# Kernel tuning notes

Hardware: AMD Instinct MI355X
Metric: run time of the kernel (lower is better)

Reference implementation:

```python
import jax, jax.numpy as jnp
import numpy as np

N_NODES = 50000
N_EDGES = 800000
IN_DIM = 96
HID_DIM = 96


def setup_inputs() -> dict:
    key = jax.random.key(0)
    ks = jax.random.split(key, 8)
    inputs = jax.random.normal(ks[0], (N_NODES, IN_DIM), dtype=jnp.float32)
    factor = jax.random.uniform(ks[1], (N_EDGES, 1), dtype=jnp.float32)
    src = jax.random.randint(ks[2], (N_EDGES,), 0, N_NODES, dtype=jnp.int32)
    dst = jax.random.randint(ks[3], (N_EDGES,), 0, N_NODES, dtype=jnp.int32)
    # Linear params (torch nn.Linear: y = x @ W.T + b), uniform(-1/sqrt(fan_in), ..)
    s1 = 1.0 / np.sqrt(IN_DIM)
    s2 = 1.0 / np.sqrt(HID_DIM)
    W1 = jax.random.uniform(ks[4], (HID_DIM, IN_DIM), minval=-s1, maxval=s1, dtype=jnp.float32)
    b1 = jax.random.uniform(ks[5], (HID_DIM,), minval=-s1, maxval=s1, dtype=jnp.float32)
    W2 = jax.random.uniform(ks[6], (IN_DIM, HID_DIM), minval=-s2, maxval=s2, dtype=jnp.float32)
    b2 = jax.random.uniform(ks[7], (IN_DIM,), minval=-s2, maxval=s2, dtype=jnp.float32)
    return {"inputs": inputs, "W1": W1, "b1": b1, "W2": W2, "b2": b2,
            "factor": factor, "src": src, "dst": dst}


def _propagate(feat, factor, src, dst, n_nodes):
    # message = h[src] * edge_factor ; reduce = sum at dst
    msg = feat[src] * factor                       # [E, D]
    return jax.ops.segment_sum(msg, dst, num_segments=n_nodes)


def reference(inputs, W1, b1, W2, b2, factor, src, dst):
    n = inputs.shape[0]
    # in-degree norm: deg^{-1/2}, clamped at 1
    deg = jax.ops.segment_sum(jnp.ones((src.shape[0],), inputs.dtype), dst,
                              num_segments=n)
    norm = jnp.maximum(deg, 1.0) ** -0.5           # [N]
    norm = norm[:, None]                           # [N, 1]

    feat = (inputs @ W1.T + b1) * norm             # [N, H]
    h = jnp.tanh(_propagate(feat, factor, src, dst, n))

    feat = (h @ W2.T + b2) * norm                  # [N, D]
    h = jnp.tanh(_propagate(feat, factor, src, dst, n))

    # dgl.mean_nodes over a single graph -> [1, D]; unsqueeze(-1) -> [1, D, 1]
    pooled = jnp.mean(h, axis=0, keepdims=True)[..., None]
    return jnp.tanh(pooled)
```

## Files before the change

### kernel.cpp

```cpp
#include <hip/hip_runtime.h>
#include <math.h>
#include <type_traits>

#define N_NODES 50000
#define N_EDGES 800000
#define DIM 96
#define BCH 12
#define SCAN_BLK 256
#define NBLK ((N_NODES + SCAN_BLK - 1) / SCAN_BLK)
#define NPB 21
#define NBG ((N_NODES + NPB - 1) / NPB)
#define CAP 768
#define R1_ROWS 24
#define R1_BLOCKS ((NBG + R1_ROWS - 1) / R1_ROWS)

typedef short v8s __attribute__((ext_vector_type(8)));
typedef float v4f __attribute__((ext_vector_type(4)));

__device__ __forceinline__ unsigned short f2bf(float f) {
    unsigned int u = __float_as_uint(f);
    u += 0x7FFFu + ((u >> 16) & 1u);
    return (unsigned short)(u >> 16);
}
__device__ __forceinline__ unsigned int pack2bf(float lo, float hi) {
    return (unsigned int)f2bf(lo) | ((unsigned int)f2bf(hi) << 16);
}
__device__ __forceinline__ float bflo(unsigned int u) { return __uint_as_float(u << 16); }
__device__ __forceinline__ float bfhi(unsigned int u) { return __uint_as_float(u & 0xFFFF0000u); }

__device__ __forceinline__ float fast_tanh(float x) {
    float ax = fabsf(x);
    float t = __expf(-2.0f * ax);
    float r = (1.0f - t) / (1.0f + t);
    return copysignf(r, x);
}

__device__ __forceinline__ void acc8(float* a, uint4 v, float f) {
    a[0] += bflo(v.x) * f; a[1] += bfhi(v.x) * f;
    a[2] += bflo(v.y) * f; a[3] += bfhi(v.y) * f;
    a[4] += bflo(v.z) * f; a[5] += bfhi(v.z) * f;
    a[6] += bflo(v.w) * f; a[7] += bfhi(v.w) * f;
}

union U4S8 { uint4 u; v8s s; };


__global__ void link_edges(const int* __restrict__ dst, int* __restrict__ head,
                           int* __restrict__ nxt) {
    int e = blockIdx.x * blockDim.x + threadIdx.x;
    if (e >= N_EDGES) return;
    int old = atomicExch(&head[dst[e]], e);
    nxt[e] = old;
}

__global__ void walk_count_partials(const int* __restrict__ head, const int* __restrict__ nxt,
                                    int* __restrict__ deg, float* __restrict__ norm,
                                    int* __restrict__ partials) {
    int b = blockIdx.x, t = threadIdx.x;
    int n = b * SCAN_BLK + t;
    int cnt = 0;
    if (n < N_NODES) {
        int p = head[n];
        while (p >= 0) { ++cnt; p = nxt[p]; }
        deg[n] = cnt;
        norm[n] = rsqrtf(fmaxf((float)cnt, 1.0f));
    }
    int v = cnt;
#pragma unroll
    for (int off = 32; off > 0; off >>= 1) v += __shfl_down(v, off, 64);
    __shared__ int ws[4];
    if ((t & 63) == 0) ws[t >> 6] = v;
    __syncthreads();
    if (t == 0) partials[b] = ws[0] + ws[1] + ws[2] + ws[3];
}

__global__ void scan_partials(const int* __restrict__ partials, int* __restrict__ pprefix) {
    __shared__ int sm[SCAN_BLK];
    int t = threadIdx.x;
    int v = (t < NBLK) ? partials[t] : 0;
    sm[t] = v;
    __syncthreads();
    for (int off = 1; off < SCAN_BLK; off <<= 1) {
        int u = (t >= off) ? sm[t - off] : 0;
        __syncthreads();
        sm[t] += u;
        __syncthreads();
    }
    if (t < NBLK) pprefix[t] = sm[t] - v;
}

__global__ void scan_compact(const int* __restrict__ deg, const int* __restrict__ pprefix,
                             const int* __restrict__ head, const int* __restrict__ nxt,
                             const int* __restrict__ src, const float* __restrict__ factor,
                             int* __restrict__ offs, int2* __restrict__ entries) {
    __shared__ int sm[SCAN_BLK];
    int b = blockIdx.x, t = threadIdx.x;
    int idx = b * SCAN_BLK + t;
    int v = (idx < N_NODES) ? deg[idx] : 0;
    sm[t] = v;
    __syncthreads();
    for (int off = 1; off < SCAN_BLK; off <<= 1) {
        int u = (t >= off) ? sm[t - off] : 0;
        __syncthreads();
        sm[t] += u;
        __syncthreads();
    }
    if (idx < N_NODES) {
        int o = pprefix[b] + sm[t] - v;
        offs[idx] = o;
        int p = head[idx];
        while (p >= 0) {
            entries[o++] = make_int2(src[p], __float_as_int(factor[p]));
            p = nxt[p];
        }
    }
    if (b == 0 && t == 0) offs[N_NODES] = N_EDGES;
}


__global__ void swizzle_W(const float* __restrict__ W, uint4* __restrict__ bsw) {
    int idx = blockIdx.x * blockDim.x + threadIdx.x;
    if (idx >= 18 * 64) return;
    int t = idx >> 6, lane = idx & 63;
    int kt = t / 6, jt = t % 6;
    int quad = lane >> 4, l16 = lane & 15;
    const float4* wp = (const float4*)(W + (size_t)(jt * 16 + l16) * DIM + kt * 32 + quad * 8);
    float4 w0 = wp[0], w1 = wp[1];
    bsw[idx] = make_uint4(pack2bf(w0.x, w0.y), pack2bf(w0.z, w0.w),
                          pack2bf(w1.x, w1.y), pack2bf(w1.z, w1.w));
}


#define TILE_SH 104

template <typename T>
__global__ __launch_bounds__(256) void gemm_mfma(const T* __restrict__ X,
                                                 const uint4* __restrict__ bsw,
                                                 const float* __restrict__ bias,
                                                 const float* __restrict__ norm,
                                                 unsigned short* __restrict__ out) {
    __shared__ unsigned short tile[4][16 * TILE_SH];
    int tid = threadIdx.x;
    int wave = tid >> 6, lane = tid & 63;
    int quad = lane >> 4, l16 = lane & 15;
    int n0 = blockIdx.x * 64 + wave * 16;
    int rowc = min(n0 + l16, N_NODES - 1);

    uint4 bfr[18];
#pragma unroll
    for (int t = 0; t < 18; ++t) bfr[t] = bsw[t * 64 + lane];

    v4f acc[6];
#pragma unroll
    for (int jt = 0; jt < 6; ++jt) acc[jt] = (v4f)(0.0f);

#pragma unroll
    for (int kt = 0; kt < 3; ++kt) {
        U4S8 a;
        if constexpr (std::is_same_v<T, float>) {
            const float4* xp = (const float4*)(X + (size_t)rowc * DIM + kt * 32 + quad * 8);
            float4 x0 = xp[0], x1 = xp[1];
            a.u = make_uint4(pack2bf(x0.x, x0.y), pack2bf(x0.z, x0.w),
                             pack2bf(x1.x, x1.y), pack2bf(x1.z, x1.w));
        } else {
            a.u = *(const uint4*)(X + (size_t)rowc * DIM + kt * 32 + quad * 8);
        }
#pragma unroll
        for (int jt = 0; jt < 6; ++jt) {
            U4S8 bb; bb.u = bfr[kt * 6 + jt];
            acc[jt] = __builtin_amdgcn_mfma_f32_16x16x32_bf16(a.s, bb.s, acc[jt], 0, 0, 0);
        }
    }

    float nm[4];
#pragma unroll
    for (int r = 0; r < 4; ++r) nm[r] = norm[min(n0 + quad * 4 + r, N_NODES - 1)];
#pragma unroll
    for (int jt = 0; jt < 6; ++jt) {
        float bj = bias[jt * 16 + l16];
#pragma unroll
        for (int r = 0; r < 4; ++r) {
            float v = (acc[jt][r] + bj) * nm[r];
            tile[wave][(quad * 4 + r) * TILE_SH + jt * 16 + l16] = f2bf(v);
        }
    }
    __builtin_amdgcn_s_waitcnt(0);
#pragma unroll
    for (int i = 0; i < 3; ++i) {
        int chunk = lane + 64 * i;
        int rr = chunk / 12, cc = chunk - rr * 12;
        int gn = n0 + rr;
        if (gn < N_NODES) {
            uint4 v = *(uint4*)&tile[wave][rr * TILE_SH + cc * 8];
            *(uint4*)(out + (size_t)gn * DIM + cc * 8) = v;
        }
    }
}


template <bool DO_TANH, bool POOL>
__global__ void gather_agg_bf16(const unsigned short* __restrict__ feat,
                                const int* __restrict__ offs,
                                const int2* __restrict__ entries,
                                unsigned short* __restrict__ out,
                                float* __restrict__ partials) {
    __shared__ int2 ents[CAP];
    __shared__ float pool[DIM];
    __shared__ int sh_base, sh_cnt;
    int tid = threadIdx.x;
    int n0 = blockIdx.x * NPB;
    int n1 = min(n0 + NPB, N_NODES);
    if (POOL && tid < DIM) pool[tid] = 0.f;
    if (tid == 0) { sh_base = offs[n0]; sh_cnt = offs[n1] - sh_base; }
    __syncthreads();
    int base = sh_base, cnt = sh_cnt;

    int nl = tid / BCH;
    int c  = tid - nl * BCH;
    int n  = n0 + nl;
    bool active = (tid < NPB * BCH) && (n < N_NODES);
    int lb = 0, le = 0;
    if (active) { lb = offs[n] - base; le = offs[n + 1] - base; }

    float a0[8], a1[8];
#pragma unroll
    for (int i = 0; i < 8; ++i) { a0[i] = 0.f; a1[i] = 0.f; }

    for (int tb = 0; tb < cnt; tb += CAP) {
        int tcnt = min(cnt - tb, CAP);
        if (tb) __syncthreads();
        for (int i = tid; i < tcnt; i += 256) ents[i] = entries[base + tb + i];
        __syncthreads();
        int s = max(lb - tb, 0), e = min(le - tb, tcnt);
        int p = s;
        for (; p + 3 < e; p += 4) {
            int2 e0 = ents[p], e1 = ents[p + 1], e2 = ents[p + 2], e3 = ents[p + 3];
            uint4 v0 = *((const uint4*)(feat + (size_t)e0.x * DIM) + c);
            uint4 v1 = *((const uint4*)(feat + (size_t)e1.x * DIM) + c);
            uint4 v2 = *((const uint4*)(feat + (size_t)e2.x * DIM) + c);
            uint4 v3 = *((const uint4*)(feat + (size_t)e3.x * DIM) + c);
            acc8(a0, v0, __int_as_float(e0.y));
            acc8(a1, v1, __int_as_float(e1.y));
            acc8(a0, v2, __int_as_float(e2.y));
            acc8(a1, v3, __int_as_float(e3.y));
        }
        for (; p < e; ++p) {
            int2 e0 = ents[p];
            uint4 v0 = *((const uint4*)(feat + (size_t)e0.x * DIM) + c);
            acc8(a0, v0, __int_as_float(e0.y));
        }
    }

#pragma unroll
    for (int i = 0; i < 8; ++i) a0[i] += a1[i];
    if (DO_TANH || POOL) {
#pragma unroll
        for (int i = 0; i < 8; ++i) a0[i] = fast_tanh(a0[i]);
    }
    if (!POOL) {
        if (active) {
            uint4 o;
            o.x = pack2bf(a0[0], a0[1]);
            o.y = pack2bf(a0[2], a0[3]);
            o.z = pack2bf(a0[4], a0[5]);
            o.w = pack2bf(a0[6], a0[7]);
            ((uint4*)out)[n * BCH + c] = o;
        }
    } else {
        if (active) {
#pragma unroll
            for (int i = 0; i < 8; ++i) atomicAdd(&pool[c * 8 + i], a0[i]);
        }
        __syncthreads();
        if (tid < DIM) partials[(size_t)blockIdx.x * DIM + tid] = pool[tid];
    }
}


__global__ void reduce_stage1(const float* __restrict__ poolpart, float* __restrict__ stage1) {
    __shared__ float pool[DIM];
    int b = blockIdx.x, t = threadIdx.x;
    if (t < DIM) pool[t] = 0.f;
    __syncthreads();
    const int base = b * R1_ROWS * DIM;
    float loc = 0.f;
    int lastc = -1;
    for (int i = t; i < R1_ROWS * DIM; i += 256) {
        int gi = base + i;
        if (gi < NBG * DIM) {
            int col = i % DIM;
            if (col != lastc) {
                if (lastc >= 0) atomicAdd(&pool[lastc], loc);
                lastc = col; loc = 0.f;
            }
            loc += poolpart[gi];
        }
    }
    if (lastc >= 0) atomicAdd(&pool[lastc], loc);
    __syncthreads();
    if (t < DIM) stage1[b * DIM + t] = pool[t];
}

__global__ void reduce_stage2(const float* __restrict__ stage1, float* __restrict__ out) {
    __shared__ float sm[960];
    int t = threadIdx.x;
    int col = t % DIM, slice = t / DIM;
    float s = 0.f;
    for (int k = slice; k < R1_BLOCKS; k += 10) s += stage1[k * DIM + col];
    sm[t] = s;
    __syncthreads();
    if (t < DIM) {
        float tot = 0.f;
#pragma unroll
        for (int i = 0; i < 10; ++i) tot += sm[i * DIM + t];
        out[t] = tanhf(tot * (1.0f / N_NODES));
    }
}


extern "C" void kernel_launch(void* const* d_in, const int* in_sizes, int n_in,
                              void* d_out, int out_size, void* d_ws, size_t ws_size,
                              hipStream_t stream) {
    const float* inputs = (const float*)d_in[0];
    const float* W1     = (const float*)d_in[1];
    const float* b1     = (const float*)d_in[2];
    const float* W2     = (const float*)d_in[3];
    const float* b2     = (const float*)d_in[4];
    const float* factor = (const float*)d_in[5];
    const int*   src    = (const int*)d_in[6];
    const int*   dst    = (const int*)d_in[7];
    float* out = (float*)d_out;

    char* ws = (char*)d_ws;
    int*            head     = (int*)(ws + 0);
    int*            nxt      = (int*)(ws + 262144);
    int*            deg      = (int*)(ws + 3670016);
    int*            offs     = (int*)(ws + 3932160);
    float*          norm     = (float*)(ws + 4194304);
    int*            partials = (int*)(ws + 4456448);
    int*            pprefix  = (int*)(ws + 4458496);
    int2*           entries  = (int2*)(ws + 4718592);
    unsigned short* bufA     = (unsigned short*)(ws + 11534336);
    unsigned short* bufB     = (unsigned short*)(ws + 21364736);
    float*          poolpart = (float*)(ws + 31195136);
    float*          stage1   = (float*)(ws + 32145536);
    uint4*          bsw1     = (uint4*)(ws + 33554432);
    uint4*          bsw2     = (uint4*)(ws + 33574912);

    swizzle_W<<<5, 256, 0, stream>>>(W1, bsw1);
    swizzle_W<<<5, 256, 0, stream>>>(W2, bsw2);

    hipMemsetAsync(head, 0xFF, N_NODES * sizeof(int), stream);
    link_edges<<<(N_EDGES + 255) / 256, 256, 0, stream>>>(dst, head, nxt);
    walk_count_partials<<<NBLK, SCAN_BLK, 0, stream>>>(head, nxt, deg, norm, partials);
    scan_partials<<<1, SCAN_BLK, 0, stream>>>(partials, pprefix);
    scan_compact<<<NBLK, SCAN_BLK, 0, stream>>>(deg, pprefix, head, nxt, src, factor,
                                                offs, entries);

    const int GEMM_BLOCKS = (N_NODES + 63) / 64;

    gemm_mfma<float><<<GEMM_BLOCKS, 256, 0, stream>>>(inputs, bsw1, b1, norm, bufA);
    gather_agg_bf16<true, false><<<NBG, 256, 0, stream>>>(bufA, offs, entries, bufB, nullptr);

    gemm_mfma<unsigned short><<<GEMM_BLOCKS, 256, 0, stream>>>(bufB, bsw2, b2, norm, bufA);
    gather_agg_bf16<false, true><<<NBG, 256, 0, stream>>>(bufA, offs, entries, nullptr, poolpart);

    reduce_stage1<<<R1_BLOCKS, 256, 0, stream>>>(poolpart, stage1);
    reduce_stage2<<<1, 960, 0, stream>>>(stage1, out);
}
```

Baseline: 265.0 us.

## Sort nodes by in-degree via histogram bins to balance gather aggregation work

Replaces the prefix-scan CSR build with a degree histogram, a per-bin scan and a rank-assignment pass. Nodes of equal in-degree become contiguous, so each gather block processes nodes with uniform edge counts. The goal is to cut divergence and idle lanes inside waves of the gather kernels. In exchange it adds a preprocessing kernel, atomic rank assignment and scattered output writes through a permutation. Degrees of 256 or more would index past the bin arrays.

```diff
diff --git a/kernel.cpp b/kernel.cpp
--- a/kernel.cpp
+++ b/kernel.cpp
@@ -11,6 +11,7 @@
 #define NPB 21
 #define NBG ((N_NODES + NPB - 1) / NPB)
 #define CAP 768
+#define NBINS 256
 #define R1_ROWS 24
 #define R1_BLOCKS ((NBG + R1_ROWS - 1) / R1_ROWS)
 
@@ -53,68 +54,74 @@
     nxt[e] = old;
 }
 
-__global__ void walk_count_partials(const int* __restrict__ head, const int* __restrict__ nxt,
-                                    int* __restrict__ deg, float* __restrict__ norm,
-                                    int* __restrict__ partials) {
-    int b = blockIdx.x, t = threadIdx.x;
-    int n = b * SCAN_BLK + t;
-    int cnt = 0;
+__global__ void walk_count_hist(const int* __restrict__ head, const int* __restrict__ nxt,
+                                int* __restrict__ deg, float* __restrict__ norm,
+                                int* __restrict__ bins) {
+    __shared__ int h[NBINS];
+    int t = threadIdx.x;
+    h[t] = 0;
+    __syncthreads();
+    int n = blockIdx.x * SCAN_BLK + t;
     if (n < N_NODES) {
+        int cnt = 0;
         int p = head[n];
         while (p >= 0) { ++cnt; p = nxt[p]; }
         deg[n] = cnt;
         norm[n] = rsqrtf(fmaxf((float)cnt, 1.0f));
-    }
-    int v = cnt;
-#pragma unroll
-    for (int off = 32; off > 0; off >>= 1) v += __shfl_down(v, off, 64);
-    __shared__ int ws[4];
-    if ((t & 63) == 0) ws[t >> 6] = v;
-    __syncthreads();
-    if (t == 0) partials[b] = ws[0] + ws[1] + ws[2] + ws[3];
-}
-
-__global__ void scan_partials(const int* __restrict__ partials, int* __restrict__ pprefix) {
-    __shared__ int sm[SCAN_BLK];
+        atomicAdd(&h[min(cnt, NBINS - 1)], 1);
+    }
+    __syncthreads();
+    if (h[t]) atomicAdd(&bins[t], h[t]);
+}
+
+__global__ void bin_scan(const int* __restrict__ bins, int* __restrict__ nodeStart,
+                         int* __restrict__ edgeStart, int* __restrict__ binCursor) {
+    __shared__ int a[NBINS], b[NBINS];
     int t = threadIdx.x;
-    int v = (t < NBLK) ? partials[t] : 0;
-    sm[t] = v;
-    __syncthreads();
-    for (int off = 1; off < SCAN_BLK; off <<= 1) {
-        int u = (t >= off) ? sm[t - off] : 0;
+    int c = bins[t];
+    int cw = c * t;
+    a[t] = c; b[t] = cw;
+    __syncthreads();
+    for (int off = 1; off < NBINS; off <<= 1) {
+        int u = (t >= off) ? a[t - off] : 0;
+        int v = (t >= off) ? b[t - off] : 0;
         __syncthreads();
-        sm[t] += u;
+        a[t] += u; b[t] += v;
         __syncthreads();
     }
-    if (t < NBLK) pprefix[t] = sm[t] - v;
-}
-
-__global__ void scan_compact(const int* __restrict__ deg, const int* __restrict__ pprefix,
-                             const int* __restrict__ head, const int* __restrict__ nxt,
-                             const int* __restrict__ src, const float* __restrict__ factor,
-                             int* __restrict__ offs, int2* __restrict__ entries) {
-    __shared__ int sm[SCAN_BLK];
-    int b = blockIdx.x, t = threadIdx.x;
-    int idx = b * SCAN_BLK + t;
-    int v = (idx < N_NODES) ? deg[idx] : 0;
-    sm[t] = v;
-    __syncthreads();
-    for (int off = 1; off < SCAN_BLK; off <<= 1) {
-        int u = (t >= off) ? sm[t - off] : 0;
-        __syncthreads();
-        sm[t] += u;
-        __syncthreads();
-    }
-    if (idx < N_NODES) {
-        int o = pprefix[b] + sm[t] - v;
-        offs[idx] = o;
-        int p = head[idx];
-        while (p >= 0) {
-            entries[o++] = make_int2(src[p], __float_as_int(factor[p]));
-            p = nxt[p];
-        }
-    }
-    if (b == 0 && t == 0) offs[N_NODES] = N_EDGES;
+    nodeStart[t] = a[t] - c;
+    edgeStart[t] = b[t] - cw;
+    binCursor[t] = 0;
+}
+
+__global__ void rank_assign(const int* __restrict__ deg, const int* __restrict__ nodeStart,
+                            const int* __restrict__ edgeStart, int* __restrict__ binCursor,
+                            int* __restrict__ perm, int* __restrict__ eoffs,
+                            int* __restrict__ soffs) {
+    int n = blockIdx.x * SCAN_BLK + threadIdx.x;
+    if (n < N_NODES) {
+        int d = deg[n];
+        int w = atomicAdd(&binCursor[d], 1);
+        int r = nodeStart[d] + w;
+        int eo = edgeStart[d] + w * d;
+        perm[r] = n;
+        eoffs[n] = eo;
+        soffs[r] = eo;
+    }
+    if (n == 0) soffs[N_NODES] = N_EDGES;
+}
+
+__global__ void compact(const int* __restrict__ head, const int* __restrict__ nxt,
+                        const int* __restrict__ src, const float* __restrict__ factor,
+                        const int* __restrict__ eoffs, int2* __restrict__ entries) {
+    int n = blockIdx.x * SCAN_BLK + threadIdx.x;
+    if (n >= N_NODES) return;
+    int o = eoffs[n];
+    int p = head[n];
+    while (p >= 0) {
+        entries[o++] = make_int2(src[p], __float_as_int(factor[p]));
+        p = nxt[p];
+    }
 }
 
 
@@ -200,7 +207,8 @@
 
 template <bool DO_TANH, bool POOL>
 __global__ void gather_agg_bf16(const unsigned short* __restrict__ feat,
-                                const int* __restrict__ offs,
+                                const int* __restrict__ soffs,
+                                const int* __restrict__ perm,
                                 const int2* __restrict__ entries,
                                 unsigned short* __restrict__ out,
                                 float* __restrict__ partials) {
@@ -208,19 +216,19 @@
     __shared__ float pool[DIM];
     __shared__ int sh_base, sh_cnt;
     int tid = threadIdx.x;
-    int n0 = blockIdx.x * NPB;
-    int n1 = min(n0 + NPB, N_NODES);
+    int r0 = blockIdx.x * NPB;
+    int r1 = min(r0 + NPB, N_NODES);
     if (POOL && tid < DIM) pool[tid] = 0.f;
-    if (tid == 0) { sh_base = offs[n0]; sh_cnt = offs[n1] - sh_base; }
+    if (tid == 0) { sh_base = soffs[r0]; sh_cnt = soffs[r1] - sh_base; }
     __syncthreads();
     int base = sh_base, cnt = sh_cnt;
 
     int nl = tid / BCH;
     int c  = tid - nl * BCH;
-    int n  = n0 + nl;
-    bool active = (tid < NPB * BCH) && (n < N_NODES);
+    int rk = r0 + nl;
+    bool active = (tid < NPB * BCH) && (rk < N_NODES);
     int lb = 0, le = 0;
-    if (active) { lb = offs[n] - base; le = offs[n + 1] - base; }
+    if (active) { lb = soffs[rk] - base; le = soffs[rk + 1] - base; }
 
     float a0[8], a1[8];
 #pragma unroll
@@ -259,12 +267,13 @@
     }
     if (!POOL) {
         if (active) {
+            int n_out = perm[rk];
             uint4 o;
             o.x = pack2bf(a0[0], a0[1]);
             o.y = pack2bf(a0[2], a0[3]);
             o.z = pack2bf(a0[4], a0[5]);
             o.w = pack2bf(a0[6], a0[7]);
-            ((uint4*)out)[n * BCH + c] = o;
+            ((uint4*)out)[n_out * BCH + c] = o;
         }
     } else {
         if (active) {
@@ -332,38 +341,46 @@
     float* out = (float*)d_out;
 
     char* ws = (char*)d_ws;
-    int*            head     = (int*)(ws + 0);
-    int*            nxt      = (int*)(ws + 262144);
-    int*            deg      = (int*)(ws + 3670016);
-    int*            offs     = (int*)(ws + 3932160);
-    float*          norm     = (float*)(ws + 4194304);
-    int*            partials = (int*)(ws + 4456448);
-    int*            pprefix  = (int*)(ws + 4458496);
-    int2*           entries  = (int2*)(ws + 4718592);
-    unsigned short* bufA     = (unsigned short*)(ws + 11534336);
-    unsigned short* bufB     = (unsigned short*)(ws + 21364736);
-    float*          poolpart = (float*)(ws + 31195136);
-    float*          stage1   = (float*)(ws + 32145536);
-    uint4*          bsw1     = (uint4*)(ws + 33554432);
-    uint4*          bsw2     = (uint4*)(ws + 33574912);
+    int*            head      = (int*)(ws + 0);
+    int*            nxt       = (int*)(ws + 262144);
+    int*            deg       = (int*)(ws + 3670016);
+    int*            soffs     = (int*)(ws + 3932160);
+    float*          norm      = (float*)(ws + 4194304);
+    int*            bins      = (int*)(ws + 4456448);
+    int*            nodeStart = (int*)(ws + 4457472);
+    int*            edgeStart = (int*)(ws + 4458496);
+    int*            binCursor = (int*)(ws + 4459520);
+    int2*           entries   = (int2*)(ws + 4718592);
+    unsigned short* bufA      = (unsigned short*)(ws + 11534336);
+    unsigned short* bufB      = (unsigned short*)(ws + 21364736);
+    float*          poolpart  = (float*)(ws + 31195136);
+    float*          stage1    = (float*)(ws + 32145536);
+    uint4*          bsw1      = (uint4*)(ws + 33554432);
+    uint4*          bsw2      = (uint4*)(ws + 33574912);
+    int*            perm      = (int*)(ws + 33595392);
+    int*            eoffs     = (int*)(ws + 33857536);
 
     swizzle_W<<<5, 256, 0, stream>>>(W1, bsw1);
     swizzle_W<<<5, 256, 0, stream>>>(W2, bsw2);
 
     hipMemsetAsync(head, 0xFF, N_NODES * sizeof(int), stream);
+    hipMemsetAsync(bins, 0, NBINS * sizeof(int), stream);
     link_edges<<<(N_EDGES + 255) / 256, 256, 0, stream>>>(dst, head, nxt);
-    walk_count_partials<<<NBLK, SCAN_BLK, 0, stream>>>(head, nxt, deg, norm, partials);
-    scan_partials<<<1, SCAN_BLK, 0, stream>>>(partials, pprefix);
-    scan_compact<<<NBLK, SCAN_BLK, 0, stream>>>(deg, pprefix, head, nxt, src, factor,
-                                                offs, entries);
+    walk_count_hist<<<NBLK, SCAN_BLK, 0, stream>>>(head, nxt, deg, norm, bins);
+    bin_scan<<<1, NBINS, 0, stream>>>(bins, nodeStart, edgeStart, binCursor);
+    rank_assign<<<NBLK, SCAN_BLK, 0, stream>>>(deg, nodeStart, edgeStart, binCursor,
+                                               perm, eoffs, soffs);
+    compact<<<NBLK, SCAN_BLK, 0, stream>>>(head, nxt, src, factor, eoffs, entries);
 
     const int GEMM_BLOCKS = (N_NODES + 63) / 64;
 
     gemm_mfma<float><<<GEMM_BLOCKS, 256, 0, stream>>>(inputs, bsw1, b1, norm, bufA);
-    gather_agg_bf16<true, false><<<NBG, 256, 0, stream>>>(bufA, offs, entries, bufB, nullptr);
+    gather_agg_bf16<true, false><<<NBG, 256, 0, stream>>>(bufA, soffs, perm, entries,
+                                                          bufB, nullptr);
 
     gemm_mfma<unsigned short><<<GEMM_BLOCKS, 256, 0, stream>>>(bufB, bsw2, b2, norm, bufA);
-    gather_agg_bf16<false, true><<<NBG, 256, 0, stream>>>(bufA, offs, entries, nullptr, poolpart);
+    gather_agg_bf16<false, true><<<NBG, 256, 0, stream>>>(bufA, soffs, perm, entries,
+                                                          nullptr, poolpart);
 
     reduce_stage1<<<R1_BLOCKS, 256, 0, stream>>>(poolpart, stage1);
     reduce_stage2<<<1, 960, 0, stream>>>(stage1, out);
```

New measurement: 393.7 us. 1.49x slower.
